# Performance work log

Hardware: AMD Instinct MI355X
Metric: run time of the kernel (lower is better)

## Reference

```python
import jax, jax.numpy as jnp
import numpy as np

EMBED_DIM = 1024
HIDDEN_DIM = 4096
NUM_EXPERTS = 8
TOP_K = 2


def setup_inputs() -> dict:
    key = jax.random.key(0)
    ks = jax.random.split(key, 5)
    x = jax.random.normal(ks[0], (2, 2048, EMBED_DIM), dtype=jnp.float32)
    Wg = jax.random.normal(ks[1], (EMBED_DIM, NUM_EXPERTS), dtype=jnp.float32) * 0.02
    W1 = jax.random.normal(ks[2], (NUM_EXPERTS, EMBED_DIM, HIDDEN_DIM), dtype=jnp.float32) * 0.02
    W3 = jax.random.normal(ks[3], (NUM_EXPERTS, EMBED_DIM, HIDDEN_DIM), dtype=jnp.float32) * 0.02
    W2 = jax.random.normal(ks[4], (NUM_EXPERTS, HIDDEN_DIM, EMBED_DIM), dtype=jnp.float32) * 0.02
    return {"x": x, "Wg": Wg, "W1": W1, "W3": W3, "W2": W2}


def reference(x, Wg, W1, W3, W2):
    # Gate: linear projection to num_experts logits
    gate = jnp.einsum("bsd,de->bse", x, Wg)  # [B,S,E]
    top_vals, top_idx = jax.lax.top_k(gate, TOP_K)  # [B,S,K]
    sel_w = jax.nn.softmax(top_vals, axis=-1)  # softmax over top-k values
    # Scatter selected weights into dense [B,S,E] (zeros for unselected experts)
    dense_w = jnp.sum(
        jax.nn.one_hot(top_idx, NUM_EXPERTS, dtype=sel_w.dtype) * sel_w[..., None],
        axis=-2,
    )  # [B,S,E]
    # Per-expert SwiGLU FFN; weight=0 for tokens not routed to expert e,
    # so the weighted-sum form is mathematically identical to masked dispatch.
    out = jnp.zeros_like(x)
    for e in range(NUM_EXPERTS):
        h = jax.nn.swish(jnp.einsum("bsd,dh->bsh", x, W1[e])) * jnp.einsum(
            "bsd,dh->bsh", x, W3[e]
        )
        out = out + dense_w[..., e:e + 1] * jnp.einsum("bsh,hd->bsd", h, W2[e])
    return out
```

## Files before the change

kernel.cpp:

```cpp
#include <hip/hip_runtime.h>
#include <hip/hip_bf16.h>
#include <stdint.h>

#define D_EMBED 1024
#define D_HID   4096
#define N_TOK   4096
#define N_EXP   8
#define CAP     4096
#define NROWA   8448

typedef __attribute__((ext_vector_type(4))) float f32x4;
typedef __attribute__((ext_vector_type(8))) short bf16x8;

__device__ __forceinline__ unsigned short f2bf(float f) {
    unsigned int u = __builtin_bit_cast(unsigned int, f);
    u += 0x7fffu + ((u >> 16) & 1u);
    return (unsigned short)(u >> 16);
}
__device__ __forceinline__ float bf2f(unsigned short h) {
    unsigned int u = ((unsigned int)h) << 16;
    return __builtin_bit_cast(float, u);
}
__device__ __forceinline__ void gload_lds16(const void* g, void* l) {
    __builtin_amdgcn_global_load_lds(
        (const __attribute__((address_space(1))) unsigned int*)g,
        (__attribute__((address_space(3))) unsigned int*)l, 16, 0, 0);
}

__global__ __launch_bounds__(256) void pack_gate(const float* __restrict__ W1,
                                                 const float* __restrict__ W3,
                                                 const float* __restrict__ W2,
                                                 const float* __restrict__ x,
                                                 const float* __restrict__ Wg,
                                                 unsigned short* __restrict__ wt13,
                                                 unsigned short* __restrict__ wt2,
                                                 int* __restrict__ counts,
                                                 int* __restrict__ toks,
                                                 float* __restrict__ wgts,
                                                 int* __restrict__ slots) {
    int b = blockIdx.x;
    if (b < 32768) {
        int idx = b * 256 + threadIdx.x;
        int pc = idx & 8191, s = (idx >> 13) & 127, e = idx >> 20;
        int g = pc >> 4;
        int rc = ((g >> 1) << 4) + (pc & 15);
        const float* src = (g & 1 ? W3 : W1) + (size_t)e * (D_EMBED * D_HID)
                         + (size_t)(s * 8) * D_HID + rc;
        bf16x8 o;
#pragma unroll
        for (int j = 0; j < 8; ++j) o[j] = (short)f2bf(src[(size_t)j * D_HID]);
        *reinterpret_cast<bf16x8*>(wt13 + (size_t)e * (D_EMBED * 2 * D_HID)
                                   + ((size_t)s * (2 * D_HID) + pc) * 8) = o;
    } else if (b < 49152) {
        int idx = (b - 32768) * 256 + threadIdx.x;
        int col = idx & 1023, s = (idx >> 10) & 511, e = idx >> 19;
        const float* src = W2 + (size_t)e * (D_HID * D_EMBED) + (size_t)(s * 8) * D_EMBED + col;
        bf16x8 o;
#pragma unroll
        for (int j = 0; j < 8; ++j) o[j] = (short)f2bf(src[(size_t)j * D_EMBED]);
        *reinterpret_cast<bf16x8*>(wt2 + (size_t)e * (D_HID * D_EMBED)
                                   + ((size_t)s * D_EMBED + col) * 8) = o;
    } else {
        int gb = b - 49152;
        int wave = threadIdx.x >> 6;
        int lane = threadIdx.x & 63;
        int tok = gb * 4 + wave;
        const float* xp = x + (size_t)tok * D_EMBED;
        float acc[8] = {0, 0, 0, 0, 0, 0, 0, 0};
#pragma unroll
        for (int i = 0; i < 16; ++i) {
            int d = lane + 64 * i;
            float xv = xp[d];
            f32x4 w0 = *reinterpret_cast<const f32x4*>(Wg + (size_t)d * 8);
            f32x4 w1 = *reinterpret_cast<const f32x4*>(Wg + (size_t)d * 8 + 4);
            acc[0] += xv * w0[0]; acc[1] += xv * w0[1]; acc[2] += xv * w0[2]; acc[3] += xv * w0[3];
            acc[4] += xv * w1[0]; acc[5] += xv * w1[1]; acc[6] += xv * w1[2]; acc[7] += xv * w1[3];
        }
#pragma unroll
        for (int e = 0; e < 8; ++e)
            for (int s = 32; s; s >>= 1) acc[e] += __shfl_xor(acc[e], s, 64);
        if (lane == 0) {
            int i0 = 0; float v0 = acc[0];
#pragma unroll
            for (int e = 1; e < 8; ++e) if (acc[e] > v0) { v0 = acc[e]; i0 = e; }
            int i1 = -1; float v1 = -1e30f;
#pragma unroll
            for (int e = 0; e < 8; ++e) if (e != i0 && acc[e] > v1) { v1 = acc[e]; i1 = e; }
            float ex = __expf(v1 - v0);
            float w0 = 1.0f / (1.0f + ex);
            float w1 = 1.0f - w0;
            int p0 = atomicAdd(&counts[i0], 1);
            toks[i0 * CAP + p0] = tok; wgts[i0 * CAP + p0] = w0; slots[i0 * CAP + p0] = 0;
            int p1 = atomicAdd(&counts[i1], 1);
            toks[i1 * CAP + p1] = tok; wgts[i1 * CAP + p1] = w1; slots[i1 * CAP + p1] = 1;
        }
    }
}

__global__ __launch_bounds__(256) void gather_x_kernel(
    const float* __restrict__ x, const int* __restrict__ counts,
    const int* __restrict__ toks, const int* __restrict__ slots,
    int* __restrict__ tok2row, unsigned short* __restrict__ xg) {
    int rt = blockIdx.x;
    int e = -1, tb = 0, osum = 0, rowbase = 0, cnt = 0, off = 0;
    for (int ee = 0; ee < N_EXP; ++ee) {
        int c = counts[ee];
        int nt = (c + 63) >> 6;
        if (rt < tb + nt) { e = ee; rowbase = (rt - tb) << 6; cnt = c; off = osum; break; }
        tb += nt; osum += c;
    }
    if (e < 0) return;
    int kb = blockIdx.y;
    int t = threadIdx.x;
    if (kb == 0 && t < 64) {
        int pos = rowbase + t;
        if (pos < cnt) {
            int i = e * CAP + pos;
            tok2row[toks[i] * 2 + slots[i]] = off + pos;
        }
    }
    __shared__ unsigned short lds[64][72];
    int r = t >> 2, ck = t & 3;
    int pos = rowbase + r;
    unsigned short tmp[16];
    if (pos < cnt) {
        int tok = toks[e * CAP + pos];
        const float* src = x + (size_t)tok * D_EMBED + kb * 64 + ck * 16;
#pragma unroll
        for (int i = 0; i < 4; ++i) {
            f32x4 v = *reinterpret_cast<const f32x4*>(src + i * 4);
#pragma unroll
            for (int j = 0; j < 4; ++j) tmp[i * 4 + j] = f2bf(v[j]);
        }
    } else {
#pragma unroll
        for (int i = 0; i < 16; ++i) tmp[i] = 0;
    }
#pragma unroll
    for (int i = 0; i < 16; ++i) lds[r][ck * 16 + i] = tmp[i];
    __syncthreads();
    int sl = t >> 5, rr = (t & 31) * 2;
#pragma unroll
    for (int w = 0; w < 2; ++w) {
        int rw = rr + w;
        if (rowbase + rw >= cnt) continue;
        bf16x8 o;
#pragma unroll
        for (int j = 0; j < 8; ++j) o[j] = (short)lds[rw][sl * 8 + j];
        *reinterpret_cast<bf16x8*>(xg + ((size_t)(kb * 8 + sl) * NROWA + off + rowbase + rw) * 8) = o;
    }
}

__global__ __launch_bounds__(256, 4) void gemm1_kernel(
    const unsigned short* __restrict__ xg,
    const unsigned short* __restrict__ wt13,
    const int* __restrict__ counts,
    const float* __restrict__ wgts,
    unsigned short* __restrict__ hp) {
    int rt = blockIdx.y;
    int e = -1, tb = 0, osum = 0, rowbase = 0, cnt = 0, off = 0;
#pragma unroll 1
    for (int ee = 0; ee < N_EXP; ++ee) {
        int c = counts[ee];
        int nt = (c + 127) >> 7;
        if (rt < tb + nt) { e = ee; rowbase = (rt - tb) << 7; cnt = c; off = osum; break; }
        tb += nt; osum += c;
    }
    if (e < 0) return;

    __shared__ __align__(16) char lds[2][16384];

    int t = threadIdx.x, lane = t & 63, w = t >> 6;
    int wr = w >> 1, wc = w & 1;
    int q = lane >> 4, p = lane & 15;

    const size_t ASTEP = (size_t)4 * NROWA * 16;
    const size_t BSTEP = (size_t)4 * (2 * D_HID) * 16;
    const size_t A2 = (size_t)2 * NROWA * 16;
    const size_t B2 = (size_t)2 * (2 * D_HID) * 16;
    const char* aS = (const char*)xg + ((size_t)(t >> 7) * NROWA + off + rowbase + (t & 127)) * 16;
    const char* bS = (const char*)wt13 + (size_t)e * D_EMBED * 2 * D_HID * 2
                   + ((size_t)(t >> 7) * (2 * D_HID) + blockIdx.x * 128 + (t & 127)) * 16;

    int wslot = 0;
    auto STG = [&]() {
        char* L = &lds[wslot][0];
        wslot ^= 1;
        gload_lds16(aS, L + t * 16);
        gload_lds16(aS + A2, L + 4096 + t * 16);
        gload_lds16(bS, L + 8192 + t * 16);
        gload_lds16(bS + B2, L + 12288 + t * 16);
        aS += ASTEP; bS += BSTEP;
    };

    f32x4 acc[4][4] = {};

    STG();
#pragma unroll 1
    for (int h = 0; h < 32; ++h) {
        if (h < 31) STG();
        if (h < 31) asm volatile("s_waitcnt vmcnt(4)" ::: "memory");
        else        asm volatile("s_waitcnt vmcnt(0)" ::: "memory");
        __builtin_amdgcn_s_barrier();
        __builtin_amdgcn_sched_barrier(0);
        const char* L = &lds[h & 1][0];
        bf16x8 af[4], bf[4];
#pragma unroll
        for (int m = 0; m < 4; ++m)
            af[m] = *reinterpret_cast<const bf16x8*>(L + (q * 128 + wr * 64 + m * 16 + p) * 16);
#pragma unroll
        for (int n = 0; n < 4; ++n)
            bf[n] = *reinterpret_cast<const bf16x8*>(L + 8192 + (q * 128 + wc * 64 + n * 16 + p) * 16);
        __builtin_amdgcn_s_setprio(1);
#pragma unroll
        for (int n = 0; n < 4; ++n)
#pragma unroll
            for (int m = 0; m < 4; ++m)
                acc[m][n] = __builtin_amdgcn_mfma_f32_16x16x32_bf16(af[m], bf[n], acc[m][n], 0, 0, 0);
        __builtin_amdgcn_s_setprio(0);
    }

#pragma unroll
    for (int m = 0; m < 4; ++m) {
#pragma unroll
        for (int reg = 0; reg < 4; ++reg) {
            int rl = wr * 64 + m * 16 + q * 4 + reg;
            int grow = rowbase + rl;
            if (grow >= cnt) continue;
            float wgt = wgts[e * CAP + grow];
            size_t row = (size_t)(off + grow);
#pragma unroll
            for (int np = 0; np < 2; ++np) {
                float a1 = acc[m][2 * np][reg];
                float a3 = acc[m][2 * np + 1][reg];
                float hv = (a1 / (1.0f + __expf(-a1))) * a3 * wgt;
                int rc = (blockIdx.x * 4 + wc * 2 + np) * 16 + p;
                hp[((size_t)(rc >> 3) * NROWA + row) * 8 + (rc & 7)] = f2bf(hv);
            }
        }
    }
}

__global__ __launch_bounds__(256, 4) void gemm2_kernel(
    const unsigned short* __restrict__ hp,
    const unsigned short* __restrict__ wt2,
    const int* __restrict__ counts,
    unsigned short* __restrict__ pbuf) {
    int rt = blockIdx.y;
    int e = -1, tb = 0, osum = 0, rowbase = 0, cnt = 0, off = 0;
#pragma unroll 1
    for (int ee = 0; ee < N_EXP; ++ee) {
        int c = counts[ee];
        int nt = (c + 127) >> 7;
        if (rt < tb + nt) { e = ee; rowbase = (rt - tb) << 7; cnt = c; off = osum; break; }
        tb += nt; osum += c;
    }
    if (e < 0) return;
    int s2 = blockIdx.z;

    __shared__ __align__(16) char lds[2][16384];

    int t = threadIdx.x, lane = t & 63, w = t >> 6;
    int wr = w >> 1, wc = w & 1;
    int q = lane >> 4, p = lane & 15;

    const size_t ASTEP = (size_t)4 * NROWA * 16;
    const size_t BSTEP = (size_t)4 * D_EMBED * 16;
    const size_t A2 = (size_t)2 * NROWA * 16;
    const size_t B2 = (size_t)2 * D_EMBED * 16;
    const char* aS = (const char*)hp
        + ((size_t)(s2 * 128 + (t >> 7)) * NROWA + off + rowbase + (t & 127)) * 16;
    const char* bS = (const char*)wt2 + (size_t)e * D_HID * D_EMBED * 2
        + ((size_t)(s2 * 128 + (t >> 7)) * D_EMBED + blockIdx.x * 128 + (t & 127)) * 16;

    int wslot = 0;
    auto STG = [&]() {
        char* L = &lds[wslot][0];
        wslot ^= 1;
        gload_lds16(aS, L + t * 16);
        gload_lds16(aS + A2, L + 4096 + t * 16);
        gload_lds16(bS, L + 8192 + t * 16);
        gload_lds16(bS + B2, L + 12288 + t * 16);
        aS += ASTEP; bS += BSTEP;
    };

    f32x4 acc[4][4] = {};

    STG();
#pragma unroll 1
    for (int h = 0; h < 32; ++h) {
        if (h < 31) STG();
        if (h < 31) asm volatile("s_waitcnt vmcnt(4)" ::: "memory");
        else        asm volatile("s_waitcnt vmcnt(0)" ::: "memory");
        __builtin_amdgcn_s_barrier();
        __builtin_amdgcn_sched_barrier(0);
        const char* L = &lds[h & 1][0];
        bf16x8 af[4], bf[4];
#pragma unroll
        for (int m = 0; m < 4; ++m)
            af[m] = *reinterpret_cast<const bf16x8*>(L + (q * 128 + wr * 64 + m * 16 + p) * 16);
#pragma unroll
        for (int n = 0; n < 4; ++n)
            bf[n] = *reinterpret_cast<const bf16x8*>(L + 8192 + (q * 128 + wc * 64 + n * 16 + p) * 16);
        __builtin_amdgcn_s_setprio(1);
#pragma unroll
        for (int n = 0; n < 4; ++n)
#pragma unroll
            for (int m = 0; m < 4; ++m)
                acc[m][n] = __builtin_amdgcn_mfma_f32_16x16x32_bf16(af[m], bf[n], acc[m][n], 0, 0, 0);
        __builtin_amdgcn_s_setprio(0);
    }

    unsigned short* pb = pbuf + (size_t)s2 * 8192 * D_EMBED;
#pragma unroll
    for (int m = 0; m < 4; ++m)
#pragma unroll
        for (int reg = 0; reg < 4; ++reg) {
            int rl = wr * 64 + m * 16 + q * 4 + reg;
            int grow = rowbase + rl;
            if (grow >= cnt) continue;
            unsigned short* dst = pb + (size_t)(off + grow) * D_EMBED + blockIdx.x * 128 + wc * 64;
#pragma unroll
            for (int n = 0; n < 4; ++n) dst[n * 16 + p] = f2bf(acc[m][n][reg]);
        }
}

__global__ __launch_bounds__(256) void combine_kernel(const unsigned short* __restrict__ pbuf,
                                                      const int* __restrict__ tok2row,
                                                      float* __restrict__ out) {
    int i = blockIdx.x * 256 + threadIdx.x;
    int tok = i >> 7, c0 = (i & 127) * 8;
    int r0 = tok2row[tok * 2], r1 = tok2row[tok * 2 + 1];
    const size_t SP = (size_t)8192 * D_EMBED;
    float s[8] = {0, 0, 0, 0, 0, 0, 0, 0};
#pragma unroll
    for (int sp = 0; sp < 4; ++sp) {
        bf16x8 a = *reinterpret_cast<const bf16x8*>(pbuf + sp * SP + (size_t)r0 * D_EMBED + c0);
        bf16x8 b = *reinterpret_cast<const bf16x8*>(pbuf + sp * SP + (size_t)r1 * D_EMBED + c0);
#pragma unroll
        for (int j = 0; j < 8; ++j)
            s[j] += bf2f((unsigned short)a[j]) + bf2f((unsigned short)b[j]);
    }
    float* op = out + (size_t)tok * D_EMBED + c0;
    f32x4 lo = {s[0], s[1], s[2], s[3]}, hi = {s[4], s[5], s[6], s[7]};
    *reinterpret_cast<f32x4*>(op) = lo;
    *reinterpret_cast<f32x4*>(op + 4) = hi;
}

extern "C" void kernel_launch(void* const* d_in, const int* in_sizes, int n_in,
                              void* d_out, int out_size, void* d_ws, size_t ws_size,
                              hipStream_t stream) {
    const float* x  = (const float*)d_in[0];
    const float* Wg = (const float*)d_in[1];
    const float* W1 = (const float*)d_in[2];
    const float* W3 = (const float*)d_in[3];
    const float* W2 = (const float*)d_in[4];
    float* out = (float*)d_out;

    char* ws = (char*)d_ws;
    size_t szW = (size_t)N_EXP * D_EMBED * D_HID;
    unsigned short* wt13 = (unsigned short*)ws; ws += szW * 2 * 2;
    unsigned short* wt2  = (unsigned short*)ws; ws += szW * 2;
    unsigned short* hp   = (unsigned short*)ws; ws += (size_t)(D_HID / 8) * NROWA * 8 * 2;
    unsigned short* xg   = (unsigned short*)ws; ws += (size_t)(D_EMBED / 8) * NROWA * 8 * 2;
    int*   toks    = (int*)ws;   ws += (size_t)N_EXP * CAP * 4;
    float* wgts    = (float*)ws; ws += (size_t)N_EXP * CAP * 4;
    int*   slots   = (int*)ws;   ws += (size_t)N_EXP * CAP * 4;
    int*   tok2row = (int*)ws;   ws += (size_t)N_TOK * 2 * 4;
    int*   counts  = (int*)ws;   ws += 8 * 4;
    unsigned short* pbuf = (unsigned short*)wt13;

    hipMemsetAsync(counts, 0, 8 * sizeof(int), stream);

    pack_gate<<<49152 + N_TOK / 4, 256, 0, stream>>>(W1, W3, W2, x, Wg, wt13, wt2,
                                                     counts, toks, wgts, slots);
    gather_x_kernel<<<dim3(136, D_EMBED / 64), 256, 0, stream>>>(x, counts, toks, slots, tok2row, xg);
    gemm1_kernel<<<dim3(64, 72), 256, 0, stream>>>(xg, wt13, counts, wgts, hp);
    gemm2_kernel<<<dim3(8, 72, 4), 256, 0, stream>>>(hp, wt2, counts, pbuf);
    combine_kernel<<<(N_TOK * 128) / 256, 256, 0, stream>>>(pbuf, tok2row, out);
}
```

Measured before the change: 472.9 us.

## Fuse fp32-to-bf16 weight conversion into GEMM B-tile loads, drop pack pass

Removes the separate pack pass that converted W1/W3/W2 to bf16 into a workspace. Both GEMMs now read fp32 weights directly, convert them in registers and write bf16 tiles to LDS. The A tiles move to a triple-buffered async global-to-LDS path, with B double-buffered through registers. This trades a full weight read-convert-write pass for redundant fp32 weight reads across row tiles, since each expert's weights are re-read once per row tile, doubling the bytes per load.

```diff
diff --git a/kernel.cpp b/kernel.cpp
--- a/kernel.cpp
+++ b/kernel.cpp
@@ -11,6 +11,7 @@
 
 typedef __attribute__((ext_vector_type(4))) float f32x4;
 typedef __attribute__((ext_vector_type(8))) short bf16x8;
+typedef __attribute__((ext_vector_type(4))) short bf16x4;
 
 __device__ __forceinline__ unsigned short f2bf(float f) {
     unsigned int u = __builtin_bit_cast(unsigned int, f);
@@ -27,73 +28,43 @@
         (__attribute__((address_space(3))) unsigned int*)l, 16, 0, 0);
 }
 
-__global__ __launch_bounds__(256) void pack_gate(const float* __restrict__ W1,
-                                                 const float* __restrict__ W3,
-                                                 const float* __restrict__ W2,
-                                                 const float* __restrict__ x,
-                                                 const float* __restrict__ Wg,
-                                                 unsigned short* __restrict__ wt13,
-                                                 unsigned short* __restrict__ wt2,
-                                                 int* __restrict__ counts,
-                                                 int* __restrict__ toks,
-                                                 float* __restrict__ wgts,
-                                                 int* __restrict__ slots) {
-    int b = blockIdx.x;
-    if (b < 32768) {
-        int idx = b * 256 + threadIdx.x;
-        int pc = idx & 8191, s = (idx >> 13) & 127, e = idx >> 20;
-        int g = pc >> 4;
-        int rc = ((g >> 1) << 4) + (pc & 15);
-        const float* src = (g & 1 ? W3 : W1) + (size_t)e * (D_EMBED * D_HID)
-                         + (size_t)(s * 8) * D_HID + rc;
-        bf16x8 o;
-#pragma unroll
-        for (int j = 0; j < 8; ++j) o[j] = (short)f2bf(src[(size_t)j * D_HID]);
-        *reinterpret_cast<bf16x8*>(wt13 + (size_t)e * (D_EMBED * 2 * D_HID)
-                                   + ((size_t)s * (2 * D_HID) + pc) * 8) = o;
-    } else if (b < 49152) {
-        int idx = (b - 32768) * 256 + threadIdx.x;
-        int col = idx & 1023, s = (idx >> 10) & 511, e = idx >> 19;
-        const float* src = W2 + (size_t)e * (D_HID * D_EMBED) + (size_t)(s * 8) * D_EMBED + col;
-        bf16x8 o;
-#pragma unroll
-        for (int j = 0; j < 8; ++j) o[j] = (short)f2bf(src[(size_t)j * D_EMBED]);
-        *reinterpret_cast<bf16x8*>(wt2 + (size_t)e * (D_HID * D_EMBED)
-                                   + ((size_t)s * D_EMBED + col) * 8) = o;
-    } else {
-        int gb = b - 49152;
-        int wave = threadIdx.x >> 6;
-        int lane = threadIdx.x & 63;
-        int tok = gb * 4 + wave;
-        const float* xp = x + (size_t)tok * D_EMBED;
-        float acc[8] = {0, 0, 0, 0, 0, 0, 0, 0};
-#pragma unroll
-        for (int i = 0; i < 16; ++i) {
-            int d = lane + 64 * i;
-            float xv = xp[d];
-            f32x4 w0 = *reinterpret_cast<const f32x4*>(Wg + (size_t)d * 8);
-            f32x4 w1 = *reinterpret_cast<const f32x4*>(Wg + (size_t)d * 8 + 4);
-            acc[0] += xv * w0[0]; acc[1] += xv * w0[1]; acc[2] += xv * w0[2]; acc[3] += xv * w0[3];
-            acc[4] += xv * w1[0]; acc[5] += xv * w1[1]; acc[6] += xv * w1[2]; acc[7] += xv * w1[3];
-        }
-#pragma unroll
-        for (int e = 0; e < 8; ++e)
-            for (int s = 32; s; s >>= 1) acc[e] += __shfl_xor(acc[e], s, 64);
-        if (lane == 0) {
-            int i0 = 0; float v0 = acc[0];
-#pragma unroll
-            for (int e = 1; e < 8; ++e) if (acc[e] > v0) { v0 = acc[e]; i0 = e; }
-            int i1 = -1; float v1 = -1e30f;
-#pragma unroll
-            for (int e = 0; e < 8; ++e) if (e != i0 && acc[e] > v1) { v1 = acc[e]; i1 = e; }
-            float ex = __expf(v1 - v0);
-            float w0 = 1.0f / (1.0f + ex);
-            float w1 = 1.0f - w0;
-            int p0 = atomicAdd(&counts[i0], 1);
-            toks[i0 * CAP + p0] = tok; wgts[i0 * CAP + p0] = w0; slots[i0 * CAP + p0] = 0;
-            int p1 = atomicAdd(&counts[i1], 1);
-            toks[i1 * CAP + p1] = tok; wgts[i1 * CAP + p1] = w1; slots[i1 * CAP + p1] = 1;
-        }
+__global__ __launch_bounds__(256) void gate_kernel(const float* __restrict__ x,
+                                                   const float* __restrict__ Wg,
+                                                   int* __restrict__ counts,
+                                                   int* __restrict__ toks,
+                                                   float* __restrict__ wgts,
+                                                   int* __restrict__ slots) {
+    int wave = threadIdx.x >> 6;
+    int lane = threadIdx.x & 63;
+    int tok = blockIdx.x * 4 + wave;
+    const float* xp = x + (size_t)tok * D_EMBED;
+    float acc[8] = {0, 0, 0, 0, 0, 0, 0, 0};
+#pragma unroll
+    for (int i = 0; i < 16; ++i) {
+        int d = lane + 64 * i;
+        float xv = xp[d];
+        f32x4 w0 = *reinterpret_cast<const f32x4*>(Wg + (size_t)d * 8);
+        f32x4 w1 = *reinterpret_cast<const f32x4*>(Wg + (size_t)d * 8 + 4);
+        acc[0] += xv * w0[0]; acc[1] += xv * w0[1]; acc[2] += xv * w0[2]; acc[3] += xv * w0[3];
+        acc[4] += xv * w1[0]; acc[5] += xv * w1[1]; acc[6] += xv * w1[2]; acc[7] += xv * w1[3];
+    }
+#pragma unroll
+    for (int e = 0; e < 8; ++e)
+        for (int s = 32; s; s >>= 1) acc[e] += __shfl_xor(acc[e], s, 64);
+    if (lane == 0) {
+        int i0 = 0; float v0 = acc[0];
+#pragma unroll
+        for (int e = 1; e < 8; ++e) if (acc[e] > v0) { v0 = acc[e]; i0 = e; }
+        int i1 = -1; float v1 = -1e30f;
+#pragma unroll
+        for (int e = 0; e < 8; ++e) if (e != i0 && acc[e] > v1) { v1 = acc[e]; i1 = e; }
+        float ex = __expf(v1 - v0);
+        float w0 = 1.0f / (1.0f + ex);
+        float w1 = 1.0f - w0;
+        int p0 = atomicAdd(&counts[i0], 1);
+        toks[i0 * CAP + p0] = tok; wgts[i0 * CAP + p0] = w0; slots[i0 * CAP + p0] = 0;
+        int p1 = atomicAdd(&counts[i1], 1);
+        toks[i1 * CAP + p1] = tok; wgts[i1 * CAP + p1] = w1; slots[i1 * CAP + p1] = 1;
     }
 }
 
@@ -153,7 +124,8 @@
 
 __global__ __launch_bounds__(256, 4) void gemm1_kernel(
     const unsigned short* __restrict__ xg,
-    const unsigned short* __restrict__ wt13,
+    const float* __restrict__ W1,
+    const float* __restrict__ W3,
     const int* __restrict__ counts,
     const float* __restrict__ wgts,
     unsigned short* __restrict__ hp) {
@@ -168,49 +140,72 @@
     }
     if (e < 0) return;
 
-    __shared__ __align__(16) char lds[2][16384];
+    __shared__ __align__(16) char lds[40960];
 
     int t = threadIdx.x, lane = t & 63, w = t >> 6;
     int wr = w >> 1, wc = w & 1;
     int q = lane >> 4, p = lane & 15;
 
     const size_t ASTEP = (size_t)4 * NROWA * 16;
-    const size_t BSTEP = (size_t)4 * (2 * D_HID) * 16;
     const size_t A2 = (size_t)2 * NROWA * 16;
-    const size_t B2 = (size_t)2 * (2 * D_HID) * 16;
     const char* aS = (const char*)xg + ((size_t)(t >> 7) * NROWA + off + rowbase + (t & 127)) * 16;
-    const char* bS = (const char*)wt13 + (size_t)e * D_EMBED * 2 * D_HID * 2
-                   + ((size_t)(t >> 7) * (2 * D_HID) + blockIdx.x * 128 + (t & 127)) * 16;
-
-    int wslot = 0;
-    auto STG = [&]() {
-        char* L = &lds[wslot][0];
-        wslot ^= 1;
+
+    int pcq = t & 31, kq = t >> 5;
+    int pcL = pcq * 4;
+    int pc  = blockIdx.x * 128 + pcL;
+    int g   = pc >> 4;
+    int rc  = ((g >> 1) << 4) + (pc & 15);
+    const float* bP = ((g & 1) ? W3 : W1) + (size_t)e * (D_EMBED * D_HID)
+                    + (size_t)(kq * 4) * D_HID + rc;
+    const size_t BSTEP = (size_t)32 * D_HID;
+    int wrel = (((kq >> 1) * 128 + pcL) * 8 + (kq & 1) * 4) * 2;
+
+    f32x4 vB[4];
+    int aw = 0, bw = 0;
+    auto BLOAD = [&]() {
+#pragma unroll
+        for (int j = 0; j < 4; ++j)
+            vB[j] = *reinterpret_cast<const f32x4*>(bP + (size_t)j * D_HID);
+        bP += BSTEP;
+    };
+    auto BWRITE = [&]() {
+        char* L = lds + 24576 + bw * 8192; bw ^= 1;
+#pragma unroll
+        for (int c = 0; c < 4; ++c) {
+            bf16x4 o = { (short)f2bf(vB[0][c]), (short)f2bf(vB[1][c]),
+                         (short)f2bf(vB[2][c]), (short)f2bf(vB[3][c]) };
+            *reinterpret_cast<bf16x4*>(L + wrel + c * 16) = o;
+        }
+    };
+    auto AGLOAD = [&]() {
+        char* L = lds + aw * 8192; aw = (aw == 2) ? 0 : aw + 1;
         gload_lds16(aS, L + t * 16);
         gload_lds16(aS + A2, L + 4096 + t * 16);
-        gload_lds16(bS, L + 8192 + t * 16);
-        gload_lds16(bS + B2, L + 12288 + t * 16);
-        aS += ASTEP; bS += BSTEP;
+        aS += ASTEP;
     };
 
     f32x4 acc[4][4] = {};
 
-    STG();
+    BLOAD(); AGLOAD();
+    BWRITE();
+    BLOAD(); AGLOAD();
+    int ar = 0;
 #pragma unroll 1
     for (int h = 0; h < 32; ++h) {
-        if (h < 31) STG();
-        if (h < 31) asm volatile("s_waitcnt vmcnt(4)" ::: "memory");
+        if (h < 31) asm volatile("s_waitcnt vmcnt(6)" ::: "memory");
         else        asm volatile("s_waitcnt vmcnt(0)" ::: "memory");
+        asm volatile("s_waitcnt lgkmcnt(0)" ::: "memory");
         __builtin_amdgcn_s_barrier();
         __builtin_amdgcn_sched_barrier(0);
-        const char* L = &lds[h & 1][0];
+        const char* LA = lds + ar * 8192; ar = (ar == 2) ? 0 : ar + 1;
+        const char* LB = lds + 24576 + (h & 1) * 8192;
         bf16x8 af[4], bf[4];
 #pragma unroll
         for (int m = 0; m < 4; ++m)
-            af[m] = *reinterpret_cast<const bf16x8*>(L + (q * 128 + wr * 64 + m * 16 + p) * 16);
+            af[m] = *reinterpret_cast<const bf16x8*>(LA + (q * 128 + wr * 64 + m * 16 + p) * 16);
 #pragma unroll
         for (int n = 0; n < 4; ++n)
-            bf[n] = *reinterpret_cast<const bf16x8*>(L + 8192 + (q * 128 + wc * 64 + n * 16 + p) * 16);
+            bf[n] = *reinterpret_cast<const bf16x8*>(LB + (q * 128 + wc * 64 + n * 16 + p) * 16);
         __builtin_amdgcn_s_setprio(1);
 #pragma unroll
         for (int n = 0; n < 4; ++n)
@@ -218,6 +213,8 @@
             for (int m = 0; m < 4; ++m)
                 acc[m][n] = __builtin_amdgcn_mfma_f32_16x16x32_bf16(af[m], bf[n], acc[m][n], 0, 0, 0);
         __builtin_amdgcn_s_setprio(0);
+        if (h < 31) BWRITE();
+        if (h < 30) { BLOAD(); AGLOAD(); }
     }
 
 #pragma unroll
@@ -234,8 +231,8 @@
                 float a1 = acc[m][2 * np][reg];
                 float a3 = acc[m][2 * np + 1][reg];
                 float hv = (a1 / (1.0f + __expf(-a1))) * a3 * wgt;
-                int rc = (blockIdx.x * 4 + wc * 2 + np) * 16 + p;
-                hp[((size_t)(rc >> 3) * NROWA + row) * 8 + (rc & 7)] = f2bf(hv);
+                int rcg = (blockIdx.x * 4 + wc * 2 + np) * 16 + p;
+                hp[((size_t)(rcg >> 3) * NROWA + row) * 8 + (rcg & 7)] = f2bf(hv);
             }
         }
     }
@@ -243,7 +240,7 @@
 
 __global__ __launch_bounds__(256, 4) void gemm2_kernel(
     const unsigned short* __restrict__ hp,
-    const unsigned short* __restrict__ wt2,
+    const float* __restrict__ W2,
     const int* __restrict__ counts,
     unsigned short* __restrict__ pbuf) {
     int rt = blockIdx.y;
@@ -258,50 +255,70 @@
     if (e < 0) return;
     int s2 = blockIdx.z;
 
-    __shared__ __align__(16) char lds[2][16384];
+    __shared__ __align__(16) char lds[40960];
 
     int t = threadIdx.x, lane = t & 63, w = t >> 6;
     int wr = w >> 1, wc = w & 1;
     int q = lane >> 4, p = lane & 15;
 
     const size_t ASTEP = (size_t)4 * NROWA * 16;
-    const size_t BSTEP = (size_t)4 * D_EMBED * 16;
     const size_t A2 = (size_t)2 * NROWA * 16;
-    const size_t B2 = (size_t)2 * D_EMBED * 16;
     const char* aS = (const char*)hp
         + ((size_t)(s2 * 128 + (t >> 7)) * NROWA + off + rowbase + (t & 127)) * 16;
-    const char* bS = (const char*)wt2 + (size_t)e * D_HID * D_EMBED * 2
-        + ((size_t)(s2 * 128 + (t >> 7)) * D_EMBED + blockIdx.x * 128 + (t & 127)) * 16;
-
-    int wslot = 0;
-    auto STG = [&]() {
-        char* L = &lds[wslot][0];
-        wslot ^= 1;
+
+    int colq = t & 31, kq = t >> 5;
+    int colL = colq * 4;
+    const float* bP = W2 + (size_t)e * (D_HID * D_EMBED)
+                    + (size_t)(s2 * 1024 + kq * 4) * D_EMBED + blockIdx.x * 128 + colL;
+    const size_t BSTEP = (size_t)32 * D_EMBED;
+    int wrel = (((kq >> 1) * 128 + colL) * 8 + (kq & 1) * 4) * 2;
+
+    f32x4 vB[4];
+    int aw = 0, bw = 0;
+    auto BLOAD = [&]() {
+#pragma unroll
+        for (int j = 0; j < 4; ++j)
+            vB[j] = *reinterpret_cast<const f32x4*>(bP + (size_t)j * D_EMBED);
+        bP += BSTEP;
+    };
+    auto BWRITE = [&]() {
+        char* L = lds + 24576 + bw * 8192; bw ^= 1;
+#pragma unroll
+        for (int c = 0; c < 4; ++c) {
+            bf16x4 o = { (short)f2bf(vB[0][c]), (short)f2bf(vB[1][c]),
+                         (short)f2bf(vB[2][c]), (short)f2bf(vB[3][c]) };
+            *reinterpret_cast<bf16x4*>(L + wrel + c * 16) = o;
+        }
+    };
+    auto AGLOAD = [&]() {
+        char* L = lds + aw * 8192; aw = (aw == 2) ? 0 : aw + 1;
         gload_lds16(aS, L + t * 16);
         gload_lds16(aS + A2, L + 4096 + t * 16);
-        gload_lds16(bS, L + 8192 + t * 16);
-        gload_lds16(bS + B2, L + 12288 + t * 16);
-        aS += ASTEP; bS += BSTEP;
+        aS += ASTEP;
     };
 
     f32x4 acc[4][4] = {};
 
-    STG();
+    BLOAD(); AGLOAD();
+    BWRITE();
+    BLOAD(); AGLOAD();
+    int ar = 0;
 #pragma unroll 1
     for (int h = 0; h < 32; ++h) {
-        if (h < 31) STG();
-        if (h < 31) asm volatile("s_waitcnt vmcnt(4)" ::: "memory");
+        if (h < 31) asm volatile("s_waitcnt vmcnt(6)" ::: "memory");
         else        asm volatile("s_waitcnt vmcnt(0)" ::: "memory");
+        asm volatile("s_waitcnt lgkmcnt(0)" ::: "memory");
         __builtin_amdgcn_s_barrier();
         __builtin_amdgcn_sched_barrier(0);
-        const char* L = &lds[h & 1][0];
+        const char* LA = lds + ar * 8192; ar = (ar == 2) ? 0 : ar + 1;
+        const char* LB = lds + 24576 + (h & 1) * 8192;
         bf16x8 af[4], bf[4];
 #pragma unroll
         for (int m = 0; m < 4; ++m)
-            af[m] = *reinterpret_cast<const bf16x8*>(L + (q * 128 + wr * 64 + m * 16 + p) * 16);
+            af[m] = *reinterpret_cast<const bf16x8*>(LA + (q * 128 + wr * 64 + m * 16 + p) * 16);
 #pragma unroll
         for (int n = 0; n < 4; ++n)
-            bf[n] = *reinterpret_cast<const bf16x8*>(L + 8192 + (q * 128 + wc * 64 + n * 16 + p) * 16);
+            bf[n] = *reinterpret_cast<const bf16x8*>(LB + (q * 128 + wc * 64 + n * 16 + p) * 16);
         __builtin_amdgcn_s_setprio(1);
 #pragma unroll
         for (int n = 0; n < 4; ++n)
@@ -309,6 +326,8 @@
             for (int m = 0; m < 4; ++m)
                 acc[m][n] = __builtin_amdgcn_mfma_f32_16x16x32_bf16(af[m], bf[n], acc[m][n], 0, 0, 0);
         __builtin_amdgcn_s_setprio(0);
+        if (h < 31) BWRITE();
+        if (h < 30) { BLOAD(); AGLOAD(); }
     }
 
     unsigned short* pb = pbuf + (size_t)s2 * 8192 * D_EMBED;
@@ -358,9 +377,7 @@
     float* out = (float*)d_out;
 
     char* ws = (char*)d_ws;
-    size_t szW = (size_t)N_EXP * D_EMBED * D_HID;
-    unsigned short* wt13 = (unsigned short*)ws; ws += szW * 2 * 2;
-    unsigned short* wt2  = (unsigned short*)ws; ws += szW * 2;
+    unsigned short* pbuf = (unsigned short*)ws; ws += (size_t)4 * 8192 * D_EMBED * 2;
     unsigned short* hp   = (unsigned short*)ws; ws += (size_t)(D_HID / 8) * NROWA * 8 * 2;
     unsigned short* xg   = (unsigned short*)ws; ws += (size_t)(D_EMBED / 8) * NROWA * 8 * 2;
     int*   toks    = (int*)ws;   ws += (size_t)N_EXP * CAP * 4;
@@ -368,14 +385,12 @@
     int*   slots   = (int*)ws;   ws += (size_t)N_EXP * CAP * 4;
     int*   tok2row = (int*)ws;   ws += (size_t)N_TOK * 2 * 4;
     int*   counts  = (int*)ws;   ws += 8 * 4;
-    unsigned short* pbuf = (unsigned short*)wt13;
 
     hipMemsetAsync(counts, 0, 8 * sizeof(int), stream);
 
-    pack_gate<<<49152 + N_TOK / 4, 256, 0, stream>>>(W1, W3, W2, x, Wg, wt13, wt2,
-                                                     counts, toks, wgts, slots);
+    gate_kernel<<<N_TOK / 4, 256, 0, stream>>>(x, Wg, counts, toks, wgts, slots);
     gather_x_kernel<<<dim3(136, D_EMBED / 64), 256, 0, stream>>>(x, counts, toks, slots, tok2row, xg);
-    gemm1_kernel<<<dim3(64, 72), 256, 0, stream>>>(xg, wt13, counts, wgts, hp);
-    gemm2_kernel<<<dim3(8, 72, 4), 256, 0, stream>>>(hp, wt2, counts, pbuf);
+    gemm1_kernel<<<dim3(64, 72), 256, 0, stream>>>(xg, W1, W3, counts, wgts, hp);
+    gemm2_kernel<<<dim3(8, 72, 4), 256, 0, stream>>>(hp, W2, counts, pbuf);
     combine_kernel<<<(N_TOK * 128) / 256, 256, 0, stream>>>(pbuf, tok2row, out);
 }
```

Result: slower. 498.3 us (+5.4%).

## Tile weight packing through LDS and halve gemm2 split-K factor

Applied to the files above, without the earlier changes.

Weight packing now reads W1/W3/W2 with coalesced float4 row loads into an LDS tile, converts to bf16, then transposes out of LDS to the k-interleaved layout, replacing the strided per-element column reads. Separately, gemm2 uses a split-K of 2 instead of 4 (64 k-steps per block), so fewer partial bf16 buffers are written and the combine kernel reads only two splits. The first targets uncoalesced global reads in the repack of about 400MB of fp32 weights. The second cuts partial-sum traffic but lowers gemm2 grid parallelism.

```diff
diff --git a/kernel.cpp b/kernel.cpp
--- a/kernel.cpp
+++ b/kernel.cpp
@@ -27,41 +27,78 @@
         (__attribute__((address_space(3))) unsigned int*)l, 16, 0, 0);
 }
 
-__global__ __launch_bounds__(256) void pack_gate(const float* __restrict__ W1,
-                                                 const float* __restrict__ W3,
-                                                 const float* __restrict__ W2,
-                                                 const float* __restrict__ x,
-                                                 const float* __restrict__ Wg,
-                                                 unsigned short* __restrict__ wt13,
-                                                 unsigned short* __restrict__ wt2,
-                                                 int* __restrict__ counts,
-                                                 int* __restrict__ toks,
-                                                 float* __restrict__ wgts,
-                                                 int* __restrict__ slots) {
+__global__ __launch_bounds__(256) void pack_gate_t(const float* __restrict__ W1,
+                                                   const float* __restrict__ W3,
+                                                   const float* __restrict__ W2,
+                                                   const float* __restrict__ x,
+                                                   const float* __restrict__ Wg,
+                                                   unsigned short* __restrict__ wt13,
+                                                   unsigned short* __restrict__ wt2,
+                                                   int* __restrict__ counts,
+                                                   int* __restrict__ toks,
+                                                   float* __restrict__ wgts,
+                                                   int* __restrict__ slots) {
     int b = blockIdx.x;
-    if (b < 32768) {
-        int idx = b * 256 + threadIdx.x;
-        int pc = idx & 8191, s = (idx >> 13) & 127, e = idx >> 20;
-        int g = pc >> 4;
-        int rc = ((g >> 1) << 4) + (pc & 15);
-        const float* src = (g & 1 ? W3 : W1) + (size_t)e * (D_EMBED * D_HID)
-                         + (size_t)(s * 8) * D_HID + rc;
-        bf16x8 o;
-#pragma unroll
-        for (int j = 0; j < 8; ++j) o[j] = (short)f2bf(src[(size_t)j * D_HID]);
-        *reinterpret_cast<bf16x8*>(wt13 + (size_t)e * (D_EMBED * 2 * D_HID)
-                                   + ((size_t)s * (2 * D_HID) + pc) * 8) = o;
-    } else if (b < 49152) {
-        int idx = (b - 32768) * 256 + threadIdx.x;
-        int col = idx & 1023, s = (idx >> 10) & 511, e = idx >> 19;
-        const float* src = W2 + (size_t)e * (D_HID * D_EMBED) + (size_t)(s * 8) * D_EMBED + col;
-        bf16x8 o;
-#pragma unroll
-        for (int j = 0; j < 8; ++j) o[j] = (short)f2bf(src[(size_t)j * D_EMBED]);
-        *reinterpret_cast<bf16x8*>(wt2 + (size_t)e * (D_HID * D_EMBED)
-                                   + ((size_t)s * D_EMBED + col) * 8) = o;
+    if (b < 16384) {
+        int cb = b & 127, kb = (b >> 7) & 15, e = b >> 11;
+        size_t ebase = (size_t)e * D_EMBED * D_HID;
+        const float* b1 = W1 + ebase + (size_t)(kb * 64) * D_HID + cb * 32;
+        const float* b3 = W3 + ebase + (size_t)(kb * 64) * D_HID + cb * 32;
+        unsigned short* op = wt13 + (size_t)e * D_EMBED * 2 * D_HID;
+        __shared__ unsigned short lds[64][72];
+        int t = threadIdx.x;
+        int r = t >> 2, ck = t & 3;
+        const float* src = (ck >= 2 ? b3 : b1) + (size_t)r * D_HID + (ck & 1) * 16;
+#pragma unroll
+        for (int i = 0; i < 2; ++i) {
+            f32x4 a = *reinterpret_cast<const f32x4*>(src + i * 8);
+            f32x4 c = *reinterpret_cast<const f32x4*>(src + i * 8 + 4);
+            bf16x8 o;
+            o[0]=(short)f2bf(a[0]); o[1]=(short)f2bf(a[1]); o[2]=(short)f2bf(a[2]); o[3]=(short)f2bf(a[3]);
+            o[4]=(short)f2bf(c[0]); o[5]=(short)f2bf(c[1]); o[6]=(short)f2bf(c[2]); o[7]=(short)f2bf(c[3]);
+            *reinterpret_cast<bf16x8*>(&lds[r][ck * 16 + i * 8]) = o;
+        }
+        __syncthreads();
+#pragma unroll
+        for (int i = 0; i < 2; ++i) {
+            int cell = i * 256 + t;
+            int ksl = cell >> 6, pcp = cell & 63;
+            int lcol = ((pcp >> 4) & 1) * 32 + ((pcp >> 5) & 1) * 16 + (pcp & 15);
+            bf16x8 o;
+#pragma unroll
+            for (int j = 0; j < 8; ++j) o[j] = (short)lds[ksl * 8 + j][lcol];
+            *reinterpret_cast<bf16x8*>(op + ((size_t)(kb * 8 + ksl) * (2 * D_HID) + cb * 64 + pcp) * 8) = o;
+        }
+    } else if (b < 24576) {
+        int bb = b - 16384;
+        int cbw = bb & 15, kb = (bb >> 4) & 63, e = bb >> 10;
+        const float* Wp = W2 + (size_t)e * D_HID * D_EMBED + (size_t)(kb * 64) * D_EMBED + cbw * 64;
+        unsigned short* op = wt2 + (size_t)e * D_HID * D_EMBED;
+        __shared__ unsigned short lds2[64][72];
+        int t = threadIdx.x;
+        int r = t >> 2, c0 = (t & 3) << 4;
+        const float* src = Wp + (size_t)r * D_EMBED + c0;
+#pragma unroll
+        for (int i = 0; i < 2; ++i) {
+            f32x4 a = *reinterpret_cast<const f32x4*>(src + i * 8);
+            f32x4 c = *reinterpret_cast<const f32x4*>(src + i * 8 + 4);
+            bf16x8 o;
+            o[0]=(short)f2bf(a[0]); o[1]=(short)f2bf(a[1]); o[2]=(short)f2bf(a[2]); o[3]=(short)f2bf(a[3]);
+            o[4]=(short)f2bf(c[0]); o[5]=(short)f2bf(c[1]); o[6]=(short)f2bf(c[2]); o[7]=(short)f2bf(c[3]);
+            *reinterpret_cast<bf16x8*>(&lds2[r][c0 + i * 8]) = o;
+        }
+        __syncthreads();
+#pragma unroll
+        for (int i = 0; i < 2; ++i) {
+            int cell = i * 256 + t;
+            int ksl = cell >> 6, col = cell & 63;
+            bf16x8 o;
+#pragma unroll
+            for (int j = 0; j < 8; ++j) o[j] = (short)lds2[ksl * 8 + j][col];
+            *reinterpret_cast<bf16x8*>(op + ((size_t)(kb * 8 + ksl) * D_EMBED + cbw * 64 + col) * 8) = o;
+        }
     } else {
-        int gb = b - 49152;
+        int gb = b - 24576;
         int wave = threadIdx.x >> 6;
         int lane = threadIdx.x & 63;
         int tok = gb * 4 + wave;
@@ -269,9 +306,9 @@
     const size_t A2 = (size_t)2 * NROWA * 16;
     const size_t B2 = (size_t)2 * D_EMBED * 16;
     const char* aS = (const char*)hp
-        + ((size_t)(s2 * 128 + (t >> 7)) * NROWA + off + rowbase + (t & 127)) * 16;
+        + ((size_t)(s2 * 256 + (t >> 7)) * NROWA + off + rowbase + (t & 127)) * 16;
     const char* bS = (const char*)wt2 + (size_t)e * D_HID * D_EMBED * 2
-        + ((size_t)(s2 * 128 + (t >> 7)) * D_EMBED + blockIdx.x * 128 + (t & 127)) * 16;
+        + ((size_t)(s2 * 256 + (t >> 7)) * D_EMBED + blockIdx.x * 128 + (t & 127)) * 16;
 
     int wslot = 0;
     auto STG = [&]() {
@@ -288,9 +325,9 @@
 
     STG();
 #pragma unroll 1
-    for (int h = 0; h < 32; ++h) {
-        if (h < 31) STG();
-        if (h < 31) asm volatile("s_waitcnt vmcnt(4)" ::: "memory");
+    for (int h = 0; h < 64; ++h) {
+        if (h < 63) STG();
+        if (h < 63) asm volatile("s_waitcnt vmcnt(4)" ::: "memory");
         else        asm volatile("s_waitcnt vmcnt(0)" ::: "memory");
         __builtin_amdgcn_s_barrier();
         __builtin_amdgcn_sched_barrier(0);
@@ -334,7 +371,7 @@
     const size_t SP = (size_t)8192 * D_EMBED;
     float s[8] = {0, 0, 0, 0, 0, 0, 0, 0};
 #pragma unroll
-    for (int sp = 0; sp < 4; ++sp) {
+    for (int sp = 0; sp < 2; ++sp) {
         bf16x8 a = *reinterpret_cast<const bf16x8*>(pbuf + sp * SP + (size_t)r0 * D_EMBED + c0);
         bf16x8 b = *reinterpret_cast<const bf16x8*>(pbuf + sp * SP + (size_t)r1 * D_EMBED + c0);
 #pragma unroll
@@ -372,10 +409,10 @@
 
     hipMemsetAsync(counts, 0, 8 * sizeof(int), stream);
 
-    pack_gate<<<49152 + N_TOK / 4, 256, 0, stream>>>(W1, W3, W2, x, Wg, wt13, wt2,
-                                                     counts, toks, wgts, slots);
+    pack_gate_t<<<25600, 256, 0, stream>>>(W1, W3, W2, x, Wg, wt13, wt2,
+                                           counts, toks, wgts, slots);
     gather_x_kernel<<<dim3(136, D_EMBED / 64), 256, 0, stream>>>(x, counts, toks, slots, tok2row, xg);
     gemm1_kernel<<<dim3(64, 72), 256, 0, stream>>>(xg, wt13, counts, wgts, hp);
-    gemm2_kernel<<<dim3(8, 72, 4), 256, 0, stream>>>(hp, wt2, counts, pbuf);
+    gemm2_kernel<<<dim3(8, 72, 2), 256, 0, stream>>>(hp, wt2, counts, pbuf);
     combine_kernel<<<(N_TOK * 128) / 256, 256, 0, stream>>>(pbuf, tok2row, out);
 }
```

Result: no change. 474.7 us (+0.4%).
